# Kernel tuning notes

Measured on AMD Instinct MI355X. Metric: run time of the kernel, lower is better.

The kernel has to match this reference:

```python
import jax, jax.numpy as jnp
import numpy as np

ALPHA = 8.3  # depth-similarity sharpness from the Depth-aware CNN paper
K = 3        # kernel size
PAD = 1      # padding (stride=1, dilation=1)


def setup_inputs() -> dict:
    key = jax.random.key(0)
    k1, k2, k3, k4 = jax.random.split(key, 4)
    B, Cin, Cout, H, W = 8, 128, 128, 128, 128
    inp = {
        "input": jax.random.normal(k1, (B, Cin, H, W), dtype=jnp.float32),
        "depth": jax.random.uniform(k2, (B, 1, H, W), dtype=jnp.float32),
        "weight": jax.random.normal(k3, (Cout, Cin, K, K), dtype=jnp.float32) * 0.05,
        "bias": jax.random.normal(k4, (Cout,), dtype=jnp.float32) * 0.05,
    }
    return inp


def reference(input, depth, weight, bias):
    # Depth-aware convolution: out(b,o,y,x) = sum_{c,kh,kw} W(o,c,kh,kw)
    #   * x(b,c,y+kh-1,x+kw-1) * exp(-ALPHA * |D(b,y,x) - D(b,y+kh-1,x+kw-1)|)
    # stride=1, dilation=1, padding=1 -> output spatial == input spatial.
    B, C, H, W = input.shape
    xp = jnp.pad(input, ((0, 0), (0, 0), (PAD, PAD), (PAD, PAD)))
    dp = jnp.pad(depth, ((0, 0), (0, 0), (PAD, PAD), (PAD, PAD)))
    acc = jnp.zeros((B, weight.shape[0], H, W), dtype=input.dtype)
    for kh in range(K):
        for kw in range(K):
            xs = xp[:, :, kh:kh + H, kw:kw + W]          # [B,C,H,W] shifted window
            ds = dp[:, :, kh:kh + H, kw:kw + W]          # [B,1,H,W]
            sim = jnp.exp(-ALPHA * jnp.abs(depth - ds))  # [B,1,H,W]
            acc = acc + jnp.einsum('bchw,oc->bohw', xs * sim, weight[:, :, kh, kw])
    return acc + bias[None, :, None, None]
```

## Files before the change

### kernel.cpp

```cpp
#include <hip/hip_runtime.h>
#include <hip/hip_bf16.h>
#include <cstdint>

#define ALPHA 8.3f

typedef __attribute__((ext_vector_type(8))) short bf16x8;
typedef __attribute__((ext_vector_type(4))) float f32x4;

__device__ __align__(16) short g_wt[9 * 128 * 128];

__device__ __forceinline__ short f2bf(float f) {
    union { float f; uint32_t u; } v; v.f = f;
    uint32_t r = v.u + 0x7fffu + ((v.u >> 16) & 1u);
    return (short)(r >> 16);
}

__global__ __launch_bounds__(256) void wt_transform(const float* __restrict__ w) {
    int tid = blockIdx.x * 256 + threadIdx.x;
    int c = tid & 127;
    int o = (tid >> 7) & 127;
    int tap = tid >> 14;
    g_wt[tid] = f2bf(w[(o * 128 + c) * 9 + tap]);
}

__global__ __launch_bounds__(256) void depthconv_main(
    const float* __restrict__ x, const float* __restrict__ depth,
    const float* __restrict__ bias, float* __restrict__ out)
{
    __shared__ __align__(16) short Atile[128 * 128];
    __shared__ float simL[9][128];
    __shared__ float dcL[128];

    const int blk = blockIdx.x;
    const int b = blk >> 7;
    const int h = blk & 127;
    const int tid = threadIdx.x;
    const int lane = tid & 63;
    const int wid = tid >> 6;
    const int wm = wid >> 1;
    const int wn = wid & 1;

    const float* xb = x + (size_t)b * (128 * 128 * 128);
    const float* db = depth + (size_t)b * (128 * 128);

    if (tid < 128) dcL[tid] = db[h * 128 + tid];
    __syncthreads();

    {
        int w = tid & 127;
        for (int tap = (tid >> 7); tap < 9; tap += 2) {
            int dh = tap / 3 - 1, dw = tap % 3 - 1;
            int hh = h + dh, ww = w + dw;
            float dsv = 0.f;
            if (hh >= 0 && hh < 128 && ww >= 0 && ww < 128) dsv = db[hh * 128 + ww];
            simL[tap][w] = __expf(-ALPHA * fabsf(dcL[w] - dsv));
        }
    }

    f32x4 acc[4][4];
    #pragma unroll
    for (int i = 0; i < 4; ++i)
        #pragma unroll
        for (int j = 0; j < 4; ++j)
            acc[i][j] = (f32x4){0.f, 0.f, 0.f, 0.f};

    const int wA = tid & 127;
    const int chalf = tid >> 7;
    char* atp = (char*)Atile;

    for (int tap = 0; tap < 9; ++tap) {
        const int dh = tap / 3 - 1, dw = tap % 3 - 1;
        const int hh = h + dh;
        if (hh < 0 || hh >= 128) continue;
        __syncthreads();

        {
            int ww = wA + dw;
            bool valid = (ww >= 0) && (ww < 128);
            int wwc = valid ? ww : 0;
            float simv = valid ? simL[tap][wA] : 0.f;
            const float* xcol = xb + (hh * 128 + wwc);
            const int swz = (wA & 7) << 4;
            #pragma unroll
            for (int oct = 0; oct < 8; ++oct) {
                int c0 = (chalf * 8 + oct) * 8;
                const float* p = xcol + (size_t)c0 * 16384;
                bf16x8 pk;
                #pragma unroll
                for (int i = 0; i < 8; ++i) {
                    float vv = p[(size_t)i * 16384] * simv;
                    pk[i] = f2bf(vv);
                }
                int byte = ((wA << 8) | (c0 << 1)) ^ swz;
                *reinterpret_cast<bf16x8*>(atp + byte) = pk;
            }
        }
        __syncthreads();

        const short* wtap = g_wt + tap * 16384;
        #pragma unroll
        for (int ks = 0; ks < 4; ++ks) {
            const int cb = ks * 32 + ((lane >> 4) << 3);
            bf16x8 bfr[4], afr[4];
            #pragma unroll
            for (int j = 0; j < 4; ++j) {
                int wrow = wn * 64 + j * 16 + (lane & 15);
                int byte = ((wrow << 8) | (cb << 1)) ^ ((wrow & 7) << 4);
                bfr[j] = *reinterpret_cast<const bf16x8*>(atp + byte);
            }
            #pragma unroll
            for (int i = 0; i < 4; ++i) {
                int orow = wm * 64 + i * 16 + (lane & 15);
                afr[i] = *reinterpret_cast<const bf16x8*>(wtap + orow * 128 + cb);
            }
            #pragma unroll
            for (int i = 0; i < 4; ++i)
                #pragma unroll
                for (int j = 0; j < 4; ++j)
                    acc[i][j] = __builtin_amdgcn_mfma_f32_16x16x32_bf16(
                        afr[i], bfr[j], acc[i][j], 0, 0, 0);
        }
    }

    #pragma unroll
    for (int i = 0; i < 4; ++i) {
        const int ob = wm * 64 + i * 16 + ((lane >> 4) << 2);
        #pragma unroll
        for (int r = 0; r < 4; ++r) {
            const int o = ob + r;
            const float bv = bias[o];
            float* orow = out + (((size_t)(b * 128 + o)) * 128 + h) * 128;
            #pragma unroll
            for (int j = 0; j < 4; ++j) {
                int w0 = wn * 64 + j * 16 + (lane & 15);
                orow[w0] = acc[i][j][r] + bv;
            }
        }
    }
}

extern "C" void kernel_launch(void* const* d_in, const int* in_sizes, int n_in,
                              void* d_out, int out_size, void* d_ws, size_t ws_size,
                              hipStream_t stream) {
    const float* x     = (const float*)d_in[0];
    const float* depth = (const float*)d_in[1];
    const float* wgt   = (const float*)d_in[2];
    const float* bias  = (const float*)d_in[3];
    float* out = (float*)d_out;

    hipLaunchKernelGGL(wt_transform, dim3(576), dim3(256), 0, stream, wgt);
    hipLaunchKernelGGL(depthconv_main, dim3(8 * 128), dim3(256), 0, stream,
                       x, depth, bias, out);
}
```

Measured before the change: 232.6 us.

## Stage 3-row input halo once in LDS and apply depth similarity post-MFMA

Each block now covers half an output row (64 pixels). It loads the three needed input rows, with halo, into LDS as bf16 a single time, instead of reloading and re-converting a shifted row for each of the 9 taps. Because the similarity factor depends only on the output pixel and tap, it is applied as a per-column scale on the per-tap MFMA partial result rather than to the input. This removes the per-tap syncs and duplicate global loads, and the grid is doubled with an occupancy hint of 3. The trade-off is extra FMA work per tap and a smaller per-wave output tile (32 output channels), which means more weight fragment loads relative to compute.

```diff
diff --git a/kernel.cpp b/kernel.cpp
--- a/kernel.cpp
+++ b/kernel.cpp
@@ -23,118 +23,127 @@
     g_wt[tid] = f2bf(w[(o * 128 + c) * 9 + tap]);
 }
 
-__global__ __launch_bounds__(256) void depthconv_main(
+__global__ __launch_bounds__(256, 3) void depthconv_main(
     const float* __restrict__ x, const float* __restrict__ depth,
     const float* __restrict__ bias, float* __restrict__ out)
 {
-    __shared__ __align__(16) short Atile[128 * 128];
-    __shared__ float simL[9][128];
-    __shared__ float dcL[128];
+    __shared__ __align__(16) short Xs[3 * 66 * 128];
+    __shared__ float simL[9][64];
 
     const int blk = blockIdx.x;
-    const int b = blk >> 7;
-    const int h = blk & 127;
+    const int b = blk >> 8;
+    const int rem = blk & 255;
+    const int h = rem >> 1;
+    const int w0 = (rem & 1) << 6;
+
     const int tid = threadIdx.x;
     const int lane = tid & 63;
     const int wid = tid >> 6;
-    const int wm = wid >> 1;
-    const int wn = wid & 1;
 
     const float* xb = x + (size_t)b * (128 * 128 * 128);
     const float* db = depth + (size_t)b * (128 * 128);
+    char* xsp = (char*)Xs;
 
-    if (tid < 128) dcL[tid] = db[h * 128 + tid];
+    for (int it = tid; it < 3168; it += 256) {
+        int r = it / 1056;
+        int rem2 = it - r * 1056;
+        int oct = rem2 / 66;
+        int wl = rem2 - oct * 66;
+        int hh = h - 1 + r;
+        int wg = w0 - 1 + wl;
+        int row = r * 66 + wl;
+        bf16x8 pk = (bf16x8){0, 0, 0, 0, 0, 0, 0, 0};
+        if (hh >= 0 && hh < 128 && wg >= 0 && wg < 128) {
+            const float* p = xb + (size_t)oct * 131072 + (size_t)hh * 128 + wg;
+            #pragma unroll
+            for (int i = 0; i < 8; ++i)
+                pk[i] = f2bf(p[(size_t)i * 16384]);
+        }
+        int byte = ((row << 8) | (oct << 4)) ^ ((row & 15) << 4);
+        *reinterpret_cast<bf16x8*>(xsp + byte) = pk;
+    }
+
+    for (int idx = tid; idx < 576; idx += 256) {
+        int t = idx >> 6;
+        int wo = idx & 63;
+        int kh = t / 3, kw = t - 3 * kh;
+        int w = w0 + wo;
+        float dc = db[h * 128 + w];
+        int hh = h + kh - 1, wg = w + kw - 1;
+        float dsv = (hh >= 0 && hh < 128 && wg >= 0 && wg < 128)
+                        ? db[hh * 128 + wg] : 0.f;
+        simL[t][wo] = __expf(-ALPHA * fabsf(dc - dsv));
+    }
     __syncthreads();
 
-    {
-        int w = tid & 127;
-        for (int tap = (tid >> 7); tap < 9; tap += 2) {
-            int dh = tap / 3 - 1, dw = tap % 3 - 1;
-            int hh = h + dh, ww = w + dw;
-            float dsv = 0.f;
-            if (hh >= 0 && hh < 128 && ww >= 0 && ww < 128) dsv = db[hh * 128 + ww];
-            simL[tap][w] = __expf(-ALPHA * fabsf(dcL[w] - dsv));
-        }
-    }
-
-    f32x4 acc[4][4];
+    f32x4 acc[2][4];
     #pragma unroll
-    for (int i = 0; i < 4; ++i)
+    for (int i = 0; i < 2; ++i)
         #pragma unroll
         for (int j = 0; j < 4; ++j)
             acc[i][j] = (f32x4){0.f, 0.f, 0.f, 0.f};
 
-    const int wA = tid & 127;
-    const int chalf = tid >> 7;
-    char* atp = (char*)Atile;
+    const int obase = wid << 5;
+    const int l15 = lane & 15;
+    const int khi = lane >> 4;
 
     for (int tap = 0; tap < 9; ++tap) {
-        const int dh = tap / 3 - 1, dw = tap % 3 - 1;
-        const int hh = h + dh;
-        if (hh < 0 || hh >= 128) continue;
-        __syncthreads();
+        const int r = tap / 3;
+        const int kw = tap - 3 * r;
+        const short* wtap = g_wt + tap * 16384;
 
-        {
-            int ww = wA + dw;
-            bool valid = (ww >= 0) && (ww < 128);
-            int wwc = valid ? ww : 0;
-            float simv = valid ? simL[tap][wA] : 0.f;
-            const float* xcol = xb + (hh * 128 + wwc);
-            const int swz = (wA & 7) << 4;
+        f32x4 P[2][4];
+        #pragma unroll
+        for (int i = 0; i < 2; ++i)
             #pragma unroll
-            for (int oct = 0; oct < 8; ++oct) {
-                int c0 = (chalf * 8 + oct) * 8;
-                const float* p = xcol + (size_t)c0 * 16384;
-                bf16x8 pk;
-                #pragma unroll
-                for (int i = 0; i < 8; ++i) {
-                    float vv = p[(size_t)i * 16384] * simv;
-                    pk[i] = f2bf(vv);
-                }
-                int byte = ((wA << 8) | (c0 << 1)) ^ swz;
-                *reinterpret_cast<bf16x8*>(atp + byte) = pk;
-            }
-        }
-        __syncthreads();
+            for (int j = 0; j < 4; ++j)
+                P[i][j] = (f32x4){0.f, 0.f, 0.f, 0.f};
 
-        const short* wtap = g_wt + tap * 16384;
         #pragma unroll
         for (int ks = 0; ks < 4; ++ks) {
-            const int cb = ks * 32 + ((lane >> 4) << 3);
-            bf16x8 bfr[4], afr[4];
+            const int cb = ks * 32 + (khi << 3);
+            bf16x8 afr[2], bfr[4];
             #pragma unroll
-            for (int j = 0; j < 4; ++j) {
-                int wrow = wn * 64 + j * 16 + (lane & 15);
-                int byte = ((wrow << 8) | (cb << 1)) ^ ((wrow & 7) << 4);
-                bfr[j] = *reinterpret_cast<const bf16x8*>(atp + byte);
-            }
-            #pragma unroll
-            for (int i = 0; i < 4; ++i) {
-                int orow = wm * 64 + i * 16 + (lane & 15);
+            for (int i = 0; i < 2; ++i) {
+                int orow = obase + i * 16 + l15;
                 afr[i] = *reinterpret_cast<const bf16x8*>(wtap + orow * 128 + cb);
             }
             #pragma unroll
-            for (int i = 0; i < 4; ++i)
+            for (int j = 0; j < 4; ++j) {
+                int wl = j * 16 + l15 + kw;
+                int row = r * 66 + wl;
+                int byte = ((row << 8) | (cb << 1)) ^ ((row & 15) << 4);
+                bfr[j] = *reinterpret_cast<const bf16x8*>(xsp + byte);
+            }
+            #pragma unroll
+            for (int i = 0; i < 2; ++i)
                 #pragma unroll
                 for (int j = 0; j < 4; ++j)
-                    acc[i][j] = __builtin_amdgcn_mfma_f32_16x16x32_bf16(
-                        afr[i], bfr[j], acc[i][j], 0, 0, 0);
+                    P[i][j] = __builtin_amdgcn_mfma_f32_16x16x32_bf16(
+                        afr[i], bfr[j], P[i][j], 0, 0, 0);
+        }
+
+        #pragma unroll
+        for (int j = 0; j < 4; ++j) {
+            float sv = simL[tap][j * 16 + l15];
+            #pragma unroll
+            for (int i = 0; i < 2; ++i)
+                #pragma unroll
+                for (int rr = 0; rr < 4; ++rr)
+                    acc[i][j][rr] += sv * P[i][j][rr];
         }
     }
 
     #pragma unroll
-    for (int i = 0; i < 4; ++i) {
-        const int ob = wm * 64 + i * 16 + ((lane >> 4) << 2);
+    for (int i = 0; i < 2; ++i) {
         #pragma unroll
-        for (int r = 0; r < 4; ++r) {
-            const int o = ob + r;
+        for (int rr = 0; rr < 4; ++rr) {
+            const int o = obase + i * 16 + (khi << 2) + rr;
             const float bv = bias[o];
-            float* orow = out + (((size_t)(b * 128 + o)) * 128 + h) * 128;
+            float* orow = out + (((size_t)(b * 128 + o)) * 128 + h) * 128 + w0;
             #pragma unroll
-            for (int j = 0; j < 4; ++j) {
-                int w0 = wn * 64 + j * 16 + (lane & 15);
-                orow[w0] = acc[i][j][r] + bv;
-            }
+            for (int j = 0; j < 4; ++j)
+                orow[j * 16 + l15] = acc[i][j][rr] + bv;
         }
     }
 }
@@ -149,6 +158,6 @@
     float* out = (float*)d_out;
 
     hipLaunchKernelGGL(wt_transform, dim3(576), dim3(256), 0, stream, wgt);
-    hipLaunchKernelGGL(depthconv_main, dim3(8 * 128), dim3(256), 0, stream,
+    hipLaunchKernelGGL(depthconv_main, dim3(8 * 128 * 2), dim3(256), 0, stream,
                        x, depth, bias, out);
 }
```

New measurement: 218.0 us. -6.3%, faster.
